# Optimization experiments

Hardware: AMD Instinct MI355X
Metric: run time of the kernel (lower is better)

The kernel has to match this reference:

```python
import jax, jax.numpy as jnp
import numpy as np

DIM = 1024
HEADS = 16
DIM_HEAD = 64
INNER = HEADS * DIM_HEAD  # 1024


def xnorm(t, gamma):
    # t * gamma / ||t||_2 along last dim (keepdims)
    norm = jnp.linalg.norm(t, ord=2, axis=-1, keepdims=True)
    return t * gamma / norm


def setup_inputs() -> dict:
    key = jax.random.key(0)
    k0, k1, k2, k3, k4 = jax.random.split(key, 5)
    x = jax.random.normal(k0, (4, 4096, DIM), dtype=jnp.float32)
    # nn.Linear weights init with std=0.001, biases zero (per init_weights)
    W_qkv = jax.random.normal(k1, (DIM, 3 * INNER), dtype=jnp.float32) * 0.001
    W_o = jax.random.normal(k2, (INNER, DIM), dtype=jnp.float32) * 0.001
    b_o = jnp.zeros((DIM,), dtype=jnp.float32)
    gamma = jax.random.normal(k3, (1, HEADS, 1, 1), dtype=jnp.float32)
    return {"x": x, "W_qkv": W_qkv, "W_o": W_o, "b_o": b_o, "gamma": gamma}


def reference(x, W_qkv, W_o, b_o, gamma):
    b, n, _ = x.shape
    qkv = x @ W_qkv  # [b, n, 3*inner]
    q, k, v = jnp.split(qkv, 3, axis=-1)
    # [b, n, h*d] -> [b, h, n, d]
    reshape_heads = lambda t: t.reshape(b, n, HEADS, DIM_HEAD).transpose(0, 2, 1, 3)
    q, k, v = map(reshape_heads, (q, k, v))
    # kv = k^T v : [b, h, d, d]
    kv = jnp.einsum('bhnd,bhne->bhde', k, v)
    kv_n = xnorm(kv, gamma)
    q_n = xnorm(q, gamma)
    out = jnp.einsum('bhnd,bhde->bhne', q_n, kv_n)  # [b, h, n, d]
    out = out.transpose(0, 2, 1, 3).reshape(b, n, INNER)
    return out @ W_o + b_o
```

## Files before the change

kernel.cpp:

```cpp
#include <hip/hip_runtime.h>


typedef __bf16 bf16;
typedef bf16  bf16x8 __attribute__((ext_vector_type(8)));
typedef bf16  bf16x4 __attribute__((ext_vector_type(4)));
typedef float f32x4  __attribute__((ext_vector_type(4)));

#define BATCH   4
#define SEQ     4096
#define DIM     1024
#define HEADS   16
#define DHEAD   64
#define MTOK    (BATCH*SEQ)
#define N_QKV   (3*DIM)
#define NSPLIT  16

#define NB_PACK (MTOK*DIM/(8*256))
#define NB_T1   ((N_QKV/32)*(DIM/32))
#define NB_T2   ((DIM/32)*(DIM/32))

typedef __attribute__((address_space(1))) const void gas_v;
typedef __attribute__((address_space(3))) void las_v;

__device__ __forceinline__ void gld_lds16(const void* g, void* l) {
  __builtin_amdgcn_global_load_lds((gas_v*)g, (las_v*)l, 16, 0, 0);
}

template <int VMN>
__device__ __forceinline__ void vmwait() {
  if constexpr (VMN == 4) asm volatile("s_waitcnt vmcnt(4)" ::: "memory");
  else if constexpr (VMN == 0) asm volatile("s_waitcnt vmcnt(0)" ::: "memory");
}

__global__ __launch_bounds__(256) void prep(const float* __restrict__ x,
                                            const float* __restrict__ Wqkv,
                                            const float* __restrict__ Wo,
                                            bf16* __restrict__ xb,
                                            bf16* __restrict__ WqT,
                                            bf16* __restrict__ WoT) {
  const int bid = blockIdx.x;
  const int t   = threadIdx.x;
  if (bid < NB_PACK) {
    size_t i = (size_t)bid * 256 + t;
    f32x4 a = *(const f32x4*)&x[i * 8];
    f32x4 b = *(const f32x4*)&x[i * 8 + 4];
    bf16x8 o = {(bf16)a.x, (bf16)a.y, (bf16)a.z, (bf16)a.w,
                (bf16)b.x, (bf16)b.y, (bf16)b.z, (bf16)b.w};
    *(bf16x8*)&xb[i * 8] = o;
    return;
  }
  __shared__ float tile[32][33];
  const float* in; bf16* out; int R, C, bx, by;
  if (bid < NB_PACK + NB_T1) {
    int tid = bid - NB_PACK;
    in = Wqkv; out = WqT; R = DIM; C = N_QKV;
    bx = tid % (N_QKV / 32); by = tid / (N_QKV / 32);
  } else {
    int tid = bid - NB_PACK - NB_T1;
    in = Wo; out = WoT; R = DIM; C = DIM;
    bx = tid & 31; by = tid >> 5;
  }
  int c0 = bx * 32, r0 = by * 32;
  int tx = t & 31, ty = t >> 5;
#pragma unroll
  for (int i = 0; i < 32; i += 8)
    tile[ty + i][tx] = in[(size_t)(r0 + ty + i) * C + c0 + tx];
  __syncthreads();
#pragma unroll
  for (int i = 0; i < 32; i += 8)
    out[(size_t)(c0 + ty + i) * R + r0 + tx] = (bf16)tile[tx][ty + i];
}

template <int MODE>
__global__ __launch_bounds__(512) void gemm256(
    const bf16* __restrict__ A, const bf16* __restrict__ Bt, int N, int K,
    float* __restrict__ C, const float* __restrict__ bias,
    const float* __restrict__ gamma,
    bf16* __restrict__ qn, bf16* __restrict__ kb, bf16* __restrict__ vb) {
  __shared__ bf16 lds[2][2][2][256 * 32];
  const int t    = threadIdx.x;
  const int lane = t & 63;
  const int wv   = t >> 6;
  const int wr   = wv >> 2;
  const int wc   = wv & 3;

  const int GX  = gridDim.x;
  const int nwg = GX * gridDim.y;
  int lin = blockIdx.y * GX + blockIdx.x;
  lin = (lin & 7) * (nwg >> 3) + (lin >> 3);
  const int m0 = (lin / GX) * 256;
  const int n0 = (lin % GX) * 256;

  const int lr   = lane & 15;
  const int ks   = lane >> 4;

  if (MODE == 2) Bt += (size_t)(m0 >> 12) * DIM * DIM;

  int aoff[8], boff[4];
#pragma unroll
  for (int i = 0; i < 8; i++) {
    int ra  = wr * 128 + i * 16 + lr;
    aoff[i] = ra * 32 + ((ks ^ ((ra >> 1) & 3)) * 8);
  }
#pragma unroll
  for (int j = 0; j < 4; j++) {
    int rb  = wc * 64 + j * 16 + lr;
    boff[j] = rb * 32 + ((ks ^ ((rb >> 1) & 3)) * 8);
  }

  const bf16* Asrc = A;
  const bf16* Bsrc = Bt;
  auto stage = [&](int op, int sl, int bufi, int tt) {
    const bf16* src = op ? Bsrc : Asrc;
    const int   rb0 = op ? n0 : m0;
    const int   k0  = tt * 64 + sl * 32;
#pragma unroll
    for (int p = 0; p < 2; ++p) {
      int row  = p * 128 + (t >> 2);
      int gseg = (t & 3) ^ ((row >> 1) & 3);
      gld_lds16(src + (size_t)(rb0 + row) * K + k0 + gseg * 8,
                &lds[bufi][op][sl][row * 32 + (t & 3) * 8]);
    }
  };

  f32x4 acc[8][4];
#pragma unroll
  for (int i = 0; i < 8; i++)
#pragma unroll
    for (int j = 0; j < 4; j++) acc[i][j] = {0.f, 0.f, 0.f, 0.f};

  bf16x8 af[4], bfv[4];

#define PH(IH, KK, BB, DOST, SOP, SSL, STT, VM)                               \
  {                                                                           \
    const bf16* sA = &lds[BB][0][KK][0];                                      \
    const bf16* sB = &lds[BB][1][KK][0];                                      \
    if ((IH) == 0) {                                                          \
      _Pragma("unroll") for (int j = 0; j < 4; j++)                           \
          bfv[j] = *(const bf16x8*)&sB[boff[j]];                              \
    }                                                                         \
    _Pragma("unroll") for (int i = 0; i < 4; i++)                             \
        af[i] = *(const bf16x8*)&sA[aoff[(IH) * 4 + i]];                      \
    if (DOST) stage(SOP, SSL, (BB) ^ 1, STT);                                 \
    vmwait<VM>();                                                             \
    __builtin_amdgcn_s_barrier();                                             \
    asm volatile("s_waitcnt lgkmcnt(0)" ::: "memory");                        \
    __builtin_amdgcn_s_setprio(1);                                            \
    _Pragma("unroll") for (int i = 0; i < 4; i++)                             \
      _Pragma("unroll") for (int j = 0; j < 4; j++)                           \
          acc[(IH) * 4 + i][j] = __builtin_amdgcn_mfma_f32_16x16x32_bf16(     \
              af[i], bfv[j], acc[(IH) * 4 + i][j], 0, 0, 0);                  \
    __builtin_amdgcn_s_setprio(0);                                            \
    __builtin_amdgcn_s_barrier();                                             \
  }

  const int NT = K >> 6;
  stage(0, 0, 0, 0); stage(1, 0, 0, 0);
  stage(0, 1, 0, 0); stage(1, 1, 0, 0);
  vmwait<4>();
  __builtin_amdgcn_s_barrier();

  for (int tt = 0; tt < NT - 1; ++tt) {
    const int bb = tt & 1;
    PH(0, 0, bb, 1, 0, 0, tt + 1, -1);
    PH(1, 0, bb, 1, 1, 0, tt + 1, 4);
    PH(0, 1, bb, 1, 0, 1, tt + 1, -1);
    PH(1, 1, bb, 1, 1, 1, tt + 1, 4);
  }
  {
    const int bb = (NT - 1) & 1;
    PH(0, 0, bb, 0, 0, 0, 0, -1);
    PH(1, 0, bb, 0, 0, 0, 0, 0);
    PH(0, 1, bb, 0, 0, 0, 0, -1);
    PH(1, 1, bb, 0, 0, 0, 0, -1);
  }
#undef PH

  const int crow0 = m0 + wr * 128 + (lane >> 4) * 4;

  if (MODE == 2) {
    const int ccol0 = n0 + wc * 64 + lr;
#pragma unroll
    for (int i = 0; i < 8; i++)
#pragma unroll
      for (int j = 0; j < 4; j++) {
        int col = ccol0 + j * 16;
#pragma unroll
        for (int r = 0; r < 4; r++)
          C[(size_t)(crow0 + i * 16 + r) * N + col] = acc[i][j][r] + bias[col];
      }
  } else {
    const int seg = n0 >> 10;
    if (seg == 0) {
      const int h    = (n0 + wc * 64) >> 6;
      const float g  = gamma[h];
      const int col0 = n0 + wc * 64 + lr;
#pragma unroll
      for (int i = 0; i < 8; i++)
#pragma unroll
        for (int r = 0; r < 4; r++) {
          float p = acc[i][0][r] * acc[i][0][r] + acc[i][1][r] * acc[i][1][r]
                  + acc[i][2][r] * acc[i][2][r] + acc[i][3][r] * acc[i][3][r];
          p += __shfl_xor(p, 1);
          p += __shfl_xor(p, 2);
          p += __shfl_xor(p, 4);
          p += __shfl_xor(p, 8);
          float sc = g * rsqrtf(p);
          size_t rb = (size_t)(crow0 + i * 16 + r) * DIM + col0;
#pragma unroll
          for (int j = 0; j < 4; j++)
            qn[rb + j * 16] = (bf16)(acc[i][j][r] * sc);
        }
    } else {
      bf16* dst = (seg == 1) ? kb : vb;
      const int ccol0 = (n0 - (seg << 10)) + wc * 64 + lr;
#pragma unroll
      for (int i = 0; i < 8; i++)
#pragma unroll
        for (int j = 0; j < 4; j++) {
          int col = ccol0 + j * 16;
#pragma unroll
          for (int r = 0; r < 4; r++)
            dst[(size_t)(crow0 + i * 16 + r) * DIM + col] = (bf16)acc[i][j][r];
        }
    }
  }
}

__global__ __launch_bounds__(256) void kv_partial(const bf16* __restrict__ kb,
                                                  const bf16* __restrict__ vb,
                                                  float* __restrict__ part) {
  __shared__ float lK[32 * 64];
  __shared__ float lV[32 * 64];
  const int t  = threadIdx.x;
  const int s  = blockIdx.x;
  const int bh = blockIdx.y;
  const int b  = bh >> 4, h = bh & 15;
  const size_t base = ((size_t)b * SEQ + s * (SEQ / NSPLIT)) * DIM + h * DHEAD;
  const int d0 = (t & 15) * 4, e0 = (t >> 4) * 4;
  const int rr = t >> 3, cc = (t & 7) * 8;

  float acc[4][4];
#pragma unroll
  for (int a = 0; a < 4; a++)
#pragma unroll
    for (int q = 0; q < 4; q++) acc[a][q] = 0.f;

  for (int nt = 0; nt < (SEQ / NSPLIT) / 32; nt++) {
    size_t g = base + (size_t)(nt * 32 + rr) * DIM + cc;
    bf16x8 k8 = *(const bf16x8*)(kb + g);
    bf16x8 v8 = *(const bf16x8*)(vb + g);
    f32x4 klo = {(float)k8[0], (float)k8[1], (float)k8[2], (float)k8[3]};
    f32x4 khi = {(float)k8[4], (float)k8[5], (float)k8[6], (float)k8[7]};
    f32x4 vlo = {(float)v8[0], (float)v8[1], (float)v8[2], (float)v8[3]};
    f32x4 vhi = {(float)v8[4], (float)v8[5], (float)v8[6], (float)v8[7]};
    *(f32x4*)&lK[rr * 64 + cc]     = klo;
    *(f32x4*)&lK[rr * 64 + cc + 4] = khi;
    *(f32x4*)&lV[rr * 64 + cc]     = vlo;
    *(f32x4*)&lV[rr * 64 + cc + 4] = vhi;
    __syncthreads();
#pragma unroll 8
    for (int nn = 0; nn < 32; nn++) {
      f32x4 kk = *(const f32x4*)&lK[nn * 64 + d0];
      f32x4 vv = *(const f32x4*)&lV[nn * 64 + e0];
#pragma unroll
      for (int a = 0; a < 4; a++)
#pragma unroll
        for (int q = 0; q < 4; q++) acc[a][q] += kk[a] * vv[q];
    }
    __syncthreads();
  }
  float* pb = part + ((size_t)bh * NSPLIT + s) * 4096;
#pragma unroll
  for (int a = 0; a < 4; a++) {
    f32x4 o = {acc[a][0], acc[a][1], acc[a][2], acc[a][3]};
    *(f32x4*)&pb[(d0 + a) * 64 + e0] = o;
  }
}

__global__ __launch_bounds__(256) void kv_norm(const float* __restrict__ part,
                                               const float* __restrict__ gamma,
                                               bf16* __restrict__ kvn) {
  const int t   = threadIdx.x;
  const int bh  = blockIdx.x >> 2;
  const int h   = bh & 15;
  const int d   = (blockIdx.x & 3) * 16 + (t >> 4);
  const int e0  = (t & 15) * 4;
  f32x4 v = {0.f, 0.f, 0.f, 0.f};
  for (int s = 0; s < NSPLIT; s++) {
    f32x4 a = *(const f32x4*)(part + ((size_t)bh * NSPLIT + s) * 4096 + d * 64 + e0);
    v.x += a.x; v.y += a.y; v.z += a.z; v.w += a.w;
  }
  float ss = v.x * v.x + v.y * v.y + v.z * v.z + v.w * v.w;
  ss += __shfl_xor(ss, 1);
  ss += __shfl_xor(ss, 2);
  ss += __shfl_xor(ss, 4);
  ss += __shfl_xor(ss, 8);
  float scale = gamma[h] * rsqrtf(ss);
  bf16x4 o = {(bf16)(v.x * scale), (bf16)(v.y * scale),
              (bf16)(v.z * scale), (bf16)(v.w * scale)};
  *(bf16x4*)&kvn[(size_t)bh * 4096 + d * 64 + e0] = o;
}

__global__ __launch_bounds__(256) void mfold(const bf16* __restrict__ WoT,
                                             const bf16* __restrict__ kvn,
                                             bf16* __restrict__ Mt) {
  __shared__ bf16 lA[128 * 64];
  __shared__ bf16 lB[64 * 64];
  const int t    = threadIdx.x;
  const int lane = t & 63;
  const int wv   = t >> 6;
  const int bh   = blockIdx.y;
  const int b    = bh >> 4, h = bh & 15;
  const int n0   = blockIdx.x * 128;

#pragma unroll
  for (int p = 0; p < 4; p++) {
    int c = p * 256 + t;
    int row = c >> 3, seg = c & 7;
    int gsk = seg ^ (row & 7);
    gld_lds16(WoT + (size_t)(n0 + row) * DIM + h * 64 + gsk * 8,
              &lA[row * 64 + seg * 8]);
  }
#pragma unroll
  for (int p = 0; p < 2; p++) {
    int c = p * 256 + t;
    int row = c >> 3, seg = c & 7;
    int gsk = seg ^ (row & 7);
    gld_lds16(kvn + (size_t)bh * 4096 + row * 64 + gsk * 8,
              &lB[row * 64 + seg * 8]);
  }
  __syncthreads();

  const int lr = lane & 15, ks = lane >> 4;
  f32x4 acc[2][4];
#pragma unroll
  for (int i = 0; i < 2; i++)
#pragma unroll
    for (int j = 0; j < 4; j++) acc[i][j] = {0.f, 0.f, 0.f, 0.f};

#pragma unroll
  for (int kk = 0; kk < 2; kk++) {
    bf16x8 af[2], bkv[4];
#pragma unroll
    for (int i = 0; i < 2; i++) {
      int row = wv * 32 + i * 16 + lr;
      int seg = (kk * 4 + ks) ^ (row & 7);
      af[i] = *(const bf16x8*)&lA[row * 64 + seg * 8];
    }
#pragma unroll
    for (int j = 0; j < 4; j++) {
      int row = j * 16 + lr;
      int seg = (kk * 4 + ks) ^ (row & 7);
      bkv[j] = *(const bf16x8*)&lB[row * 64 + seg * 8];
    }
#pragma unroll
    for (int i = 0; i < 2; i++)
#pragma unroll
      for (int j = 0; j < 4; j++)
        acc[i][j] = __builtin_amdgcn_mfma_f32_16x16x32_bf16(af[i], bkv[j],
                                                            acc[i][j], 0, 0, 0);
  }

  bf16* mb = Mt + (size_t)b * DIM * DIM;
#pragma unroll
  for (int i = 0; i < 2; i++)
#pragma unroll
    for (int j = 0; j < 4; j++) {
      int col = h * 64 + j * 16 + lr;
#pragma unroll
      for (int r = 0; r < 4; r++) {
        int row = n0 + wv * 32 + i * 16 + ks * 4 + r;
        mb[(size_t)row * DIM + col] = (bf16)acc[i][j][r];
      }
    }
}

extern "C" void kernel_launch(void* const* d_in, const int* in_sizes, int n_in,
                              void* d_out, int out_size, void* d_ws,
                              size_t ws_size, hipStream_t stream) {
  const float* x     = (const float*)d_in[0];
  const float* Wqkv  = (const float*)d_in[1];
  const float* Wo    = (const float*)d_in[2];
  const float* bo    = (const float*)d_in[3];
  const float* gamma = (const float*)d_in[4];
  float* out = (float*)d_out;

  char* ws = (char*)d_ws;
  size_t off = 0;
  bf16*  xb   = (bf16*)(ws + off);  off += (size_t)MTOK * DIM * 2;
  bf16*  WqT  = (bf16*)(ws + off);  off += (size_t)N_QKV * DIM * 2;
  bf16*  WoT  = (bf16*)(ws + off);  off += (size_t)DIM * DIM * 2;
  bf16*  kvn  = (bf16*)(ws + off);  off += (size_t)64 * 4096 * 2;
  bf16*  qn   = (bf16*)(ws + off);  off += (size_t)MTOK * DIM * 2;
  bf16*  kb   = (bf16*)(ws + off);  off += (size_t)MTOK * DIM * 2;
  bf16*  vb   = (bf16*)(ws + off);  off += (size_t)MTOK * DIM * 2;
  float* part = (float*)(ws + off); off += (size_t)64 * NSPLIT * 4096 * 4;
  bf16*  Mt   = (bf16*)(ws + off);  off += (size_t)BATCH * DIM * DIM * 2;

  prep<<<dim3(NB_PACK + NB_T1 + NB_T2), dim3(256), 0, stream>>>(
      x, Wqkv, Wo, xb, WqT, WoT);

  gemm256<1><<<dim3(N_QKV / 256, MTOK / 256), dim3(512), 0, stream>>>(
      xb, WqT, N_QKV, DIM, nullptr, nullptr, gamma, qn, kb, vb);

  kv_partial<<<dim3(NSPLIT, 64), dim3(256), 0, stream>>>(kb, vb, part);
  kv_norm<<<dim3(256), dim3(256), 0, stream>>>(part, gamma, kvn);

  mfold<<<dim3(DIM / 128, 64), dim3(256), 0, stream>>>(WoT, kvn, Mt);

  gemm256<2><<<dim3(DIM / 256, MTOK / 256), dim3(512), 0, stream>>>(
      qn, Mt, DIM, DIM, out, bo, nullptr, nullptr, nullptr, nullptr);
}
```

Baseline: 326.6 us.

## Shrink GEMM tile to 256x128 with triple-buffered single-barrier K loop

Both GEMMs now use a 256x128 output tile instead of 256x256. Each of the 8 waves computes a 64x64 sub-tile, and the launch grid doubles along N. The K loop switches from double-buffered 64-wide steps with two barriers per phase to a 3-stage ring of 32-wide stages with one barrier each, and launch bounds request higher occupancy. The aim is to cut accumulator register pressure, raise occupancy and wave count, and lower barrier overhead. In exchange, A-tile reuse per loaded B element drops and more global and LDS traffic is spent per FLOP.

```diff
diff --git a/kernel.cpp b/kernel.cpp
--- a/kernel.cpp
+++ b/kernel.cpp
@@ -28,7 +28,7 @@
 
 template <int VMN>
 __device__ __forceinline__ void vmwait() {
-  if constexpr (VMN == 4) asm volatile("s_waitcnt vmcnt(4)" ::: "memory");
+  if constexpr (VMN == 3)      asm volatile("s_waitcnt vmcnt(3)" ::: "memory");
   else if constexpr (VMN == 0) asm volatile("s_waitcnt vmcnt(0)" ::: "memory");
 }
 
@@ -72,34 +72,35 @@
 }
 
 template <int MODE>
-__global__ __launch_bounds__(512) void gemm256(
+__global__ __launch_bounds__(512, 4) void gemm256(
     const bf16* __restrict__ A, const bf16* __restrict__ Bt, int N, int K,
     float* __restrict__ C, const float* __restrict__ bias,
     const float* __restrict__ gamma,
     bf16* __restrict__ qn, bf16* __restrict__ kb, bf16* __restrict__ vb) {
-  __shared__ bf16 lds[2][2][2][256 * 32];
+  __shared__ bf16 lA[3][256 * 32];
+  __shared__ bf16 lB[3][128 * 32];
   const int t    = threadIdx.x;
   const int lane = t & 63;
   const int wv   = t >> 6;
-  const int wr   = wv >> 2;
-  const int wc   = wv & 3;
+  const int wr   = wv >> 1;
+  const int wc   = wv & 1;
 
   const int GX  = gridDim.x;
   const int nwg = GX * gridDim.y;
   int lin = blockIdx.y * GX + blockIdx.x;
   lin = (lin & 7) * (nwg >> 3) + (lin >> 3);
   const int m0 = (lin / GX) * 256;
-  const int n0 = (lin % GX) * 256;
+  const int n0 = (lin % GX) * 128;
 
   const int lr   = lane & 15;
   const int ks   = lane >> 4;
 
   if (MODE == 2) Bt += (size_t)(m0 >> 12) * DIM * DIM;
 
-  int aoff[8], boff[4];
-#pragma unroll
-  for (int i = 0; i < 8; i++) {
-    int ra  = wr * 128 + i * 16 + lr;
+  int aoff[4], boff[4];
+#pragma unroll
+  for (int i = 0; i < 4; i++) {
+    int ra  = wr * 64 + i * 16 + lr;
     aoff[i] = ra * 32 + ((ks ^ ((ra >> 1) & 3)) * 8);
   }
 #pragma unroll
@@ -110,78 +111,72 @@
 
   const bf16* Asrc = A;
   const bf16* Bsrc = Bt;
-  auto stage = [&](int op, int sl, int bufi, int tt) {
-    const bf16* src = op ? Bsrc : Asrc;
-    const int   rb0 = op ? n0 : m0;
-    const int   k0  = tt * 64 + sl * 32;
+  auto stage = [&](int bufi, int tt) {
+    const int k0 = tt << 5;
 #pragma unroll
     for (int p = 0; p < 2; ++p) {
       int row  = p * 128 + (t >> 2);
       int gseg = (t & 3) ^ ((row >> 1) & 3);
-      gld_lds16(src + (size_t)(rb0 + row) * K + k0 + gseg * 8,
-                &lds[bufi][op][sl][row * 32 + (t & 3) * 8]);
+      gld_lds16(Asrc + (size_t)(m0 + row) * K + k0 + gseg * 8,
+                &lA[bufi][row * 32 + (t & 3) * 8]);
+    }
+    {
+      int row  = t >> 2;
+      int gseg = (t & 3) ^ ((row >> 1) & 3);
+      gld_lds16(Bsrc + (size_t)(n0 + row) * K + k0 + gseg * 8,
+                &lB[bufi][row * 32 + (t & 3) * 8]);
     }
   };
 
-  f32x4 acc[8][4];
-#pragma unroll
-  for (int i = 0; i < 8; i++)
+  f32x4 acc[4][4];
+#pragma unroll
+  for (int i = 0; i < 4; i++)
 #pragma unroll
     for (int j = 0; j < 4; j++) acc[i][j] = {0.f, 0.f, 0.f, 0.f};
 
   bf16x8 af[4], bfv[4];
 
-#define PH(IH, KK, BB, DOST, SOP, SSL, STT, VM)                               \
+#define PH(TB, DOST, SB, STT, VM)                                             \
   {                                                                           \
-    const bf16* sA = &lds[BB][0][KK][0];                                      \
-    const bf16* sB = &lds[BB][1][KK][0];                                      \
-    if ((IH) == 0) {                                                          \
-      _Pragma("unroll") for (int j = 0; j < 4; j++)                           \
-          bfv[j] = *(const bf16x8*)&sB[boff[j]];                              \
-    }                                                                         \
+    const bf16* sA = &lA[TB][0];                                              \
+    const bf16* sB = &lB[TB][0];                                              \
+    _Pragma("unroll") for (int j = 0; j < 4; j++)                             \
+        bfv[j] = *(const bf16x8*)&sB[boff[j]];                                \
     _Pragma("unroll") for (int i = 0; i < 4; i++)                             \
-        af[i] = *(const bf16x8*)&sA[aoff[(IH) * 4 + i]];                      \
-    if (DOST) stage(SOP, SSL, (BB) ^ 1, STT);                                 \
+        af[i] = *(const bf16x8*)&sA[aoff[i]];                                 \
+    if (DOST) stage(SB, STT);                                                 \
     vmwait<VM>();                                                             \
     __builtin_amdgcn_s_barrier();                                             \
     asm volatile("s_waitcnt lgkmcnt(0)" ::: "memory");                        \
     __builtin_amdgcn_s_setprio(1);                                            \
     _Pragma("unroll") for (int i = 0; i < 4; i++)                             \
       _Pragma("unroll") for (int j = 0; j < 4; j++)                           \
-          acc[(IH) * 4 + i][j] = __builtin_amdgcn_mfma_f32_16x16x32_bf16(     \
-              af[i], bfv[j], acc[(IH) * 4 + i][j], 0, 0, 0);                  \
+          acc[i][j] = __builtin_amdgcn_mfma_f32_16x16x32_bf16(                \
+              af[i], bfv[j], acc[i][j], 0, 0, 0);                             \
     __builtin_amdgcn_s_setprio(0);                                            \
-    __builtin_amdgcn_s_barrier();                                             \
-  }
-
-  const int NT = K >> 6;
-  stage(0, 0, 0, 0); stage(1, 0, 0, 0);
-  stage(0, 1, 0, 0); stage(1, 1, 0, 0);
-  vmwait<4>();
+  }
+
+  const int NT = K >> 5;
+  stage(0, 0);
+  stage(1, 1);
+  vmwait<3>();
   __builtin_amdgcn_s_barrier();
 
-  for (int tt = 0; tt < NT - 1; ++tt) {
-    const int bb = tt & 1;
-    PH(0, 0, bb, 1, 0, 0, tt + 1, -1);
-    PH(1, 0, bb, 1, 1, 0, tt + 1, 4);
-    PH(0, 1, bb, 1, 0, 1, tt + 1, -1);
-    PH(1, 1, bb, 1, 1, 1, tt + 1, 4);
-  }
-  {
-    const int bb = (NT - 1) & 1;
-    PH(0, 0, bb, 0, 0, 0, 0, -1);
-    PH(1, 0, bb, 0, 0, 0, 0, 0);
-    PH(0, 1, bb, 0, 0, 0, 0, -1);
-    PH(1, 1, bb, 0, 0, 0, 0, -1);
-  }
+  for (int tt = 0; tt < NT - 2; tt += 3) {
+    PH(0, 1, 2, tt + 2, 3);
+    PH(1, 1, 0, tt + 3, 3);
+    PH(2, 1, 1, tt + 4, 3);
+  }
+  PH(0, 0, 0, 0, 0);
+  PH(1, 0, 0, 0, -1);
 #undef PH
 
-  const int crow0 = m0 + wr * 128 + (lane >> 4) * 4;
+  const int crow0 = m0 + wr * 64 + (lane >> 4) * 4;
 
   if (MODE == 2) {
     const int ccol0 = n0 + wc * 64 + lr;
 #pragma unroll
-    for (int i = 0; i < 8; i++)
+    for (int i = 0; i < 4; i++)
 #pragma unroll
       for (int j = 0; j < 4; j++) {
         int col = ccol0 + j * 16;
@@ -196,7 +191,7 @@
       const float g  = gamma[h];
       const int col0 = n0 + wc * 64 + lr;
 #pragma unroll
-      for (int i = 0; i < 8; i++)
+      for (int i = 0; i < 4; i++)
 #pragma unroll
         for (int r = 0; r < 4; r++) {
           float p = acc[i][0][r] * acc[i][0][r] + acc[i][1][r] * acc[i][1][r]
@@ -215,7 +210,7 @@
       bf16* dst = (seg == 1) ? kb : vb;
       const int ccol0 = (n0 - (seg << 10)) + wc * 64 + lr;
 #pragma unroll
-      for (int i = 0; i < 8; i++)
+      for (int i = 0; i < 4; i++)
 #pragma unroll
         for (int j = 0; j < 4; j++) {
           int col = ccol0 + j * 16;
@@ -401,7 +396,7 @@
   prep<<<dim3(NB_PACK + NB_T1 + NB_T2), dim3(256), 0, stream>>>(
       x, Wqkv, Wo, xb, WqT, WoT);
 
-  gemm256<1><<<dim3(N_QKV / 256, MTOK / 256), dim3(512), 0, stream>>>(
+  gemm256<1><<<dim3(N_QKV / 128, MTOK / 256), dim3(512), 0, stream>>>(
       xb, WqT, N_QKV, DIM, nullptr, nullptr, gamma, qn, kb, vb);
 
   kv_partial<<<dim3(NSPLIT, 64), dim3(256), 0, stream>>>(kb, vb, part);
@@ -409,6 +404,6 @@
 
   mfold<<<dim3(DIM / 128, 64), dim3(256), 0, stream>>>(WoT, kvn, Mt);
 
-  gemm256<2><<<dim3(DIM / 256, MTOK / 256), dim3(512), 0, stream>>>(
+  gemm256<2><<<dim3(DIM / 128, MTOK / 256), dim3(512), 0, stream>>>(
       qn, Mt, DIM, DIM, out, bo, nullptr, nullptr, nullptr, nullptr);
 }
```

Result: no change. 324.9 us (-0.5%).
